# Performance work log

Hardware: AMD Instinct MI355X
Metric: run time of the kernel (lower is better)

Reference implementation:

```python
import jax, jax.numpy as jnp
import numpy as np

B, S, D = 4, 4096, 2048
H, DH = 16, 128
ROPE_BASE = 10000.0


def rotate_half(x):
    x1, x2 = jnp.split(x, 2, axis=-1)
    return jnp.concatenate((-x2, x1), axis=-1)


def rope_cos_sin(seq_len, head_dim, dtype):
    inv_freq = 1.0 / (ROPE_BASE ** (jnp.arange(0, head_dim, 2, dtype=jnp.float32) / head_dim))
    pos = jnp.arange(seq_len, dtype=jnp.float32)
    freqs = pos[:, None] * inv_freq[None, :]          # [S, DH/2]
    emb = jnp.concatenate((freqs, freqs), axis=-1)    # [S, DH]
    return jnp.cos(emb).astype(dtype), jnp.sin(emb).astype(dtype)


def setup_inputs() -> dict:
    key = jax.random.key(0)
    ks = jax.random.split(key, 5)
    scale = 0.02
    return {
        "hidden_states": jax.random.normal(ks[0], (B, S, D), jnp.float32),
        "Wq": jax.random.normal(ks[1], (D, D), jnp.float32) * scale,
        "Wk": jax.random.normal(ks[2], (D, D), jnp.float32) * scale,
        "Wv": jax.random.normal(ks[3], (D, D), jnp.float32) * scale,
        "Wo": jax.random.normal(ks[4], (D, D), jnp.float32) * scale,
    }


def reference(hidden_states, Wq, Wk, Wv, Wo):
    b, s, d = hidden_states.shape
    # QKV projections (nn.Linear stores weight as [out, in] -> x @ W.T)
    def proj(W):
        y = hidden_states @ W.T                       # [B, S, D]
        return y.reshape(b, s, H, DH).transpose(0, 2, 1, 3)  # [B, H, S, DH]
    q, k, v = proj(Wq), proj(Wk), proj(Wv)

    # RoPE (cos/sin broadcast over head dim: unsqueeze_dim=1)
    cos, sin = rope_cos_sin(s, DH, hidden_states.dtype)  # [S, DH]
    cos = cos[None, None]                                # [1, 1, S, DH]
    sin = sin[None, None]
    q = q * cos + rotate_half(q) * sin
    k = k * cos + rotate_half(k) * sin

    # SDPA, non-causal, no mask, eval mode (dropout 0)
    scale = 1.0 / jnp.sqrt(jnp.asarray(DH, hidden_states.dtype))
    scores = jnp.einsum("bhqd,bhkd->bhqk", q, k) * scale
    attn = jax.nn.softmax(scores, axis=-1)
    ctx = jnp.einsum("bhqk,bhkd->bhqd", attn, v)         # [B, H, S, DH]

    ctx = ctx.transpose(0, 2, 1, 3).reshape(b, s, H * DH)
    return ctx @ Wo.T
```

## Files before the change

kernel.cpp:

```cpp
#include <hip/hip_runtime.h>
#include <hip/hip_bf16.h>
#include <math.h>

typedef __attribute__((ext_vector_type(4)))  float f32x4;
typedef __attribute__((ext_vector_type(16))) float f32x16;
typedef __attribute__((ext_vector_type(8)))  short s16x8;
typedef __attribute__((ext_vector_type(4)))  short s16x4;
typedef __attribute__((ext_vector_type(4)))  int   i32x4;

#define DEVI __device__ __forceinline__


DEVI unsigned short f2bf(float x) {
    unsigned int u = __builtin_bit_cast(unsigned int, x);
    u += 0x7fffu + ((u >> 16) & 1u);
    return (unsigned short)(u >> 16);
}

DEVI f32x4 mfma16(s16x8 a, s16x8 b, f32x4 c) {
    return __builtin_amdgcn_mfma_f32_16x16x32_bf16(a, b, c, 0, 0, 0);
}
DEVI f32x16 mfma32(s16x8 a, s16x8 b, f32x16 c) {
    return __builtin_amdgcn_mfma_f32_32x32x16_bf16(a, b, c, 0, 0, 0);
}
DEVI int cvtpk(float lo, float hi) {
    int r; asm("v_cvt_pk_bf16_f32 %0, %1, %2" : "=v"(r) : "v"(lo), "v"(hi)); return r;
}
DEVI void plswap(int& a, int& b) {
    asm volatile("v_permlane32_swap_b32 %0, %1" : "+v"(a), "+v"(b));
}
DEVI void gload16(const void* g, void* l) {
    __builtin_amdgcn_global_load_lds(
        (const __attribute__((address_space(1))) void*)g,
        (__attribute__((address_space(3))) void*)l, 16, 0, 0);
}

__global__ __launch_bounds__(256)
void cvt_kernel(const float* __restrict__ in, unsigned short* __restrict__ out, int n8) {
    int i = blockIdx.x * 256 + threadIdx.x;
    const int stride = gridDim.x * 256;
    for (; i < n8; i += stride) {
        f32x4 a = ((const f32x4*)in)[i * 2];
        f32x4 b = ((const f32x4*)in)[i * 2 + 1];
        s16x8 o;
#pragma unroll
        for (int e = 0; e < 4; ++e) o[e] = (short)f2bf(a[e]);
#pragma unroll
        for (int e = 0; e < 4; ++e) o[4 + e] = (short)f2bf(b[e]);
        *(s16x8*)&out[(size_t)i * 8] = o;
    }
}

__global__ void rope_table_kernel(float* __restrict__ cosb, float* __restrict__ sinb) {
    const int s = blockIdx.x;
    const int i = threadIdx.x;
    const float inv = expf(-(float)i * (9.210340371976184f / 64.0f));
    const float ang = (float)s * inv;
    cosb[s * 64 + i] = cosf(ang);
    sinb[s * 64 + i] = sinf(ang);
}

template <int EPI>
__global__ __launch_bounds__(512, 1)
void gemm8_kernel(const unsigned short* __restrict__ Ah,
                  const unsigned short* __restrict__ Wh,
                  void* __restrict__ Cp, const float* __restrict__ cosb,
                  const float* __restrict__ sinb, float oscale)
{
    constexpr int KD = 2048;
    __shared__ __align__(16) char smem[98304];

    const int tid  = threadIdx.x;
    const int lane = tid & 63;
    const int wid  = tid >> 6;
    const int wm   = wid >> 1;
    const int wn   = wid & 1;
    const int lr   = lane & 15;
    const int lkg  = lane >> 4;
    const int m0   = blockIdx.x * 256;
    const int n0   = blockIdx.y * 128;

    const f32x4 zero4 = {0.f, 0.f, 0.f, 0.f};
    f32x4 acc[4][4];
#pragma unroll
    for (int i = 0; i < 4; ++i)
#pragma unroll
        for (int j = 0; j < 4; ++j) acc[i][j] = zero4;

    const int rsw = (lkg ^ ((lr >> 1) & 3)) << 4;

    auto stageA = [&](int b, int t, int kh) {
        const int k0 = t * 64 + kh * 32;
        char* dst = smem + b * 49152 + kh * 16384;
#pragma unroll
        for (int c = 0; c < 2; ++c) {
            int flat = c * 512 + tid;
            int row  = flat >> 2, slot = flat & 3;
            int sg   = slot ^ ((row >> 1) & 3);
            gload16(&Ah[(size_t)(m0 + row) * KD + k0 + sg * 8], dst + flat * 16);
        }
    };
    auto stageB = [&](int b, int t, int kh) {
        const int k0 = t * 64 + kh * 32;
        char* dst = smem + b * 49152 + 32768 + kh * 8192;
        int row = tid >> 2, slot = tid & 3;
        int sg  = slot ^ ((row >> 1) & 3);
        gload16(&Wh[(size_t)(n0 + row) * KD + k0 + sg * 8], dst + tid * 16);
    };

    auto phase = [&](int b, int ks) {
        const char* Ab = smem + b * 49152 + ks * 16384;
        const char* Bb = smem + b * 49152 + 32768 + ks * 8192;
        s16x8 af[4], bf[4];
#pragma unroll
        for (int mi = 0; mi < 4; ++mi) {
            int row = wm * 64 + mi * 16 + lr;
            af[mi] = *(const s16x8*)(Ab + row * 64 + rsw);
        }
#pragma unroll
        for (int nj = 0; nj < 4; ++nj) {
            int row = wn * 32 + (nj & 1) * 16 + (nj >> 1) * 64 + lr;
            bf[nj] = *(const s16x8*)(Bb + row * 64 + rsw);
        }
        __builtin_amdgcn_s_setprio(1);
#pragma unroll
        for (int mi = 0; mi < 4; ++mi)
#pragma unroll
            for (int nj = 0; nj < 4; ++nj)
                acc[mi][nj] = mfma16(af[mi], bf[nj], acc[mi][nj]);
        __builtin_amdgcn_s_setprio(0);
    };

    stageA(0, 0, 0); stageB(0, 0, 0);
    stageA(0, 0, 1); stageB(0, 0, 1);
    asm volatile("s_waitcnt vmcnt(0)" ::: "memory");
    __builtin_amdgcn_s_barrier();

    for (int t = 0; t < 31; ++t) {
        const int b = t & 1;
        stageA(b ^ 1, t + 1, 0); stageB(b ^ 1, t + 1, 0);
        phase(b, 0);
        asm volatile("s_waitcnt vmcnt(3)" ::: "memory");
        __builtin_amdgcn_s_barrier();
        stageA(b ^ 1, t + 1, 1); stageB(b ^ 1, t + 1, 1);
        phase(b, 1);
        asm volatile("s_waitcnt vmcnt(3)" ::: "memory");
        __builtin_amdgcn_s_barrier();
    }
    phase(1, 0);
    asm volatile("s_waitcnt vmcnt(0)" ::: "memory");
    __builtin_amdgcn_s_barrier();
    phase(1, 1);

    if constexpr (EPI == 0) {
        unsigned short* Qb = (unsigned short*)Cp;
        const int h = blockIdx.y;
#pragma unroll
        for (int mi = 0; mi < 4; ++mi) {
#pragma unroll
            for (int reg = 0; reg < 4; ++reg) {
                int mg = m0 + wm * 64 + mi * 16 + lkg * 4 + reg;
                int bb = mg >> 12, s = mg & 4095;
                size_t base = ((size_t)(bb * 16 + h) * 4096 + s) * 128;
#pragma unroll
                for (int nj = 0; nj < 2; ++nj) {
                    int dlo = wn * 32 + nj * 16 + lr;
                    float cv = cosb[s * 64 + dlo];
                    float sv = sinb[s * 64 + dlo];
                    float a  = acc[mi][nj][reg];
                    float b2 = acc[mi][nj + 2][reg];
                    Qb[base + dlo]      = f2bf((a * cv - b2 * sv) * oscale);
                    Qb[base + dlo + 64] = f2bf((b2 * cv + a * sv) * oscale);
                }
            }
        }
    } else if constexpr (EPI == 1) {
        unsigned short* Vt = (unsigned short*)Cp;
        const int h = blockIdx.y;
        unsigned short* Cs = (unsigned short*)smem;
        __syncthreads();
#pragma unroll
        for (int mi = 0; mi < 4; ++mi)
#pragma unroll
            for (int nj = 0; nj < 4; ++nj) {
                int col = wn * 32 + (nj & 1) * 16 + (nj >> 1) * 64 + lr;
#pragma unroll
                for (int reg = 0; reg < 4; ++reg) {
                    int row = wm * 64 + mi * 16 + lkg * 4 + reg;
                    Cs[row * 136 + col] = f2bf(acc[mi][nj][reg]);
                }
            }
        __syncthreads();
        const int dh = tid >> 2;
        const int sh = (tid & 3) * 64;
        const int bb = m0 >> 12, sbase = m0 & 4095;
        size_t gbase = ((size_t)((bb * 16 + h) * 128 + dh)) * 4096 + sbase + sh;
#pragma unroll
        for (int j0 = 0; j0 < 8; ++j0) {
            s16x8 v;
#pragma unroll
            for (int e = 0; e < 8; ++e)
                v[e] = (short)Cs[(sh + j0 * 8 + e) * 136 + dh];
            *(s16x8*)&Vt[gbase + j0 * 8] = v;
        }
    } else {
        float* Ob = (float*)Cp;
#pragma unroll
        for (int mi = 0; mi < 4; ++mi)
#pragma unroll
            for (int reg = 0; reg < 4; ++reg) {
                int mg = m0 + wm * 64 + mi * 16 + lkg * 4 + reg;
#pragma unroll
                for (int nj = 0; nj < 4; ++nj) {
                    int col = n0 + wn * 32 + (nj & 1) * 16 + (nj >> 1) * 64 + lr;
                    Ob[(size_t)mg * 2048 + col] = acc[mi][nj][reg];
                }
            }
    }
}

template <bool AB16, int EPI>
__global__ __launch_bounds__(256, 2)
void gemm_kernel(const void* __restrict__ Ap, const float* __restrict__ Bw,
                 void* __restrict__ Cp, const float* __restrict__ cosb,
                 const float* __restrict__ sinb, float oscale)
{
    constexpr int KD = 2048;
    __shared__ __align__(16) unsigned short smem[20480];
    unsigned short* const As = smem;
    unsigned short* const Bs = smem + 10240;

    const int tid  = threadIdx.x;
    const int lane = tid & 63;
    const int wid  = tid >> 6;
    const int wr   = wid >> 1, wc = wid & 1;
    const int lr   = lane & 15;
    const int lkg  = lane >> 4;
    const int lk   = lkg * 8;
    const int m0   = blockIdx.x * 128;
    const int n0   = blockIdx.y * 128;

    const f32x4 zero4 = {0.f, 0.f, 0.f, 0.f};
    f32x4 acc[4][4];
#pragma unroll
    for (int i = 0; i < 4; ++i)
#pragma unroll
        for (int j = 0; j < 4; ++j) acc[i][j] = zero4;

    f32x4 aF[4], bF[4];
    s16x8 aH[2];
    const float* Af = (const float*)Ap;
    const unsigned short* AhL = (const unsigned short*)Ap;

    auto stage_load = [&](int kt) {
        const int k0 = kt * 32;
        if constexpr (!AB16) {
#pragma unroll
            for (int i = 0; i < 4; ++i) {
                int flat = i * 256 + tid;
                int r = flat >> 3, c = (flat & 7) * 4;
                aF[i] = *(const f32x4*)&Af[(size_t)(m0 + r) * KD + k0 + c];
            }
        } else {
#pragma unroll
            for (int i = 0; i < 2; ++i) {
                int flat = i * 256 + tid;
                int r = flat >> 2, c = (flat & 3) * 8;
                aH[i] = *(const s16x8*)&AhL[(size_t)(m0 + r) * KD + k0 + c];
            }
        }
#pragma unroll
        for (int i = 0; i < 4; ++i) {
            int flat = i * 256 + tid;
            int r = flat >> 3, c = (flat & 7) * 4;
            bF[i] = *(const f32x4*)&Bw[(size_t)(n0 + r) * KD + k0 + c];
        }
    };
    auto stage_write = [&](int buf) {
        unsigned short* Ab = As + buf * 5120;
        unsigned short* Bb = Bs + buf * 5120;
        if constexpr (!AB16) {
#pragma unroll
            for (int i = 0; i < 4; ++i) {
                int flat = i * 256 + tid;
                int r = flat >> 3, c = (flat & 7) * 4;
                s16x4 v;
#pragma unroll
                for (int e = 0; e < 4; ++e) v[e] = (short)f2bf(aF[i][e]);
                *(s16x4*)&Ab[r * 40 + c] = v;
            }
        } else {
#pragma unroll
            for (int i = 0; i < 2; ++i) {
                int flat = i * 256 + tid;
                int r = flat >> 2, c = (flat & 3) * 8;
                *(s16x8*)&Ab[r * 40 + c] = aH[i];
            }
        }
#pragma unroll
        for (int i = 0; i < 4; ++i) {
            int flat = i * 256 + tid;
            int r = flat >> 3, c = (flat & 7) * 4;
            s16x4 v;
#pragma unroll
            for (int e = 0; e < 4; ++e) v[e] = (short)f2bf(bF[i][e]);
            *(s16x4*)&Bb[r * 40 + c] = v;
        }
    };
    const int ncol0 = wc * 32;
    auto compute = [&](int buf) {
        const unsigned short* Ab = As + buf * 5120;
        const unsigned short* Bb = Bs + buf * 5120;
        s16x8 af[4], bf[4];
#pragma unroll
        for (int mi = 0; mi < 4; ++mi)
            af[mi] = *(const s16x8*)&Ab[(wr * 64 + mi * 16 + lr) * 40 + lk];
#pragma unroll
        for (int nj = 0; nj < 4; ++nj) {
            int nc = ncol0 + (nj & 1) * 16 + (nj >> 1) * 64;
            bf[nj] = *(const s16x8*)&Bb[(nc + lr) * 40 + lk];
        }
#pragma unroll
        for (int mi = 0; mi < 4; ++mi)
#pragma unroll
            for (int nj = 0; nj < 4; ++nj)
                acc[mi][nj] = mfma16(af[mi], bf[nj], acc[mi][nj]);
    };
    stage_load(0);
    stage_write(0);
    __syncthreads();
    for (int kt = 0; kt < 64; ++kt) {
        const int cur = kt & 1;
        if (kt < 63) stage_load(kt + 1);
        compute(cur);
        if (kt < 63) stage_write(cur ^ 1);
        __syncthreads();
    }

    if constexpr (EPI == 0) {
        unsigned short* Qb = (unsigned short*)Cp;
        const int h = blockIdx.y;
#pragma unroll
        for (int mi = 0; mi < 4; ++mi) {
#pragma unroll
            for (int reg = 0; reg < 4; ++reg) {
                int mg = m0 + wr * 64 + mi * 16 + lkg * 4 + reg;
                int bb = mg >> 12, s = mg & 4095;
                size_t base = ((size_t)(bb * 16 + h) * 4096 + s) * 128;
#pragma unroll
                for (int nj = 0; nj < 2; ++nj) {
                    int dlo = wc * 32 + nj * 16 + lr;
                    float cv = cosb[s * 64 + dlo];
                    float sv = sinb[s * 64 + dlo];
                    float a  = acc[mi][nj][reg];
                    float b2 = acc[mi][nj + 2][reg];
                    Qb[base + dlo]      = f2bf((a * cv - b2 * sv) * oscale);
                    Qb[base + dlo + 64] = f2bf((b2 * cv + a * sv) * oscale);
                }
            }
        }
    } else if constexpr (EPI == 1) {
        unsigned short* Vt = (unsigned short*)Cp;
        const int h = blockIdx.y;
        unsigned short* Cs = smem;
        __syncthreads();
#pragma unroll
        for (int mi = 0; mi < 4; ++mi)
#pragma unroll
            for (int nj = 0; nj < 4; ++nj) {
                int col = wc * 32 + (nj & 1) * 16 + (nj >> 1) * 64 + lr;
#pragma unroll
                for (int reg = 0; reg < 4; ++reg) {
                    int row = wr * 64 + mi * 16 + lkg * 4 + reg;
                    Cs[row * 136 + col] = f2bf(acc[mi][nj][reg]);
                }
            }
        __syncthreads();
        const int dh = tid >> 1;
        const int sh = (tid & 1) * 64;
        const int bb = m0 >> 12, sbase = m0 & 4095;
        size_t gbase = ((size_t)((bb * 16 + h) * 128 + dh)) * 4096 + sbase + sh;
#pragma unroll
        for (int j0 = 0; j0 < 8; ++j0) {
            s16x8 v;
#pragma unroll
            for (int e = 0; e < 8; ++e)
                v[e] = (short)Cs[(sh + j0 * 8 + e) * 136 + dh];
            *(s16x8*)&Vt[gbase + j0 * 8] = v;
        }
    } else {
        float* Ob = (float*)Cp;
#pragma unroll
        for (int mi = 0; mi < 4; ++mi)
#pragma unroll
            for (int reg = 0; reg < 4; ++reg) {
                int mg = m0 + wr * 64 + mi * 16 + lkg * 4 + reg;
#pragma unroll
                for (int nj = 0; nj < 4; ++nj) {
                    int col = n0 + wc * 32 + (nj & 1) * 16 + (nj >> 1) * 64 + lr;
                    Ob[(size_t)mg * 2048 + col] = acc[mi][nj][reg];
                }
            }
    }
}

__global__ __launch_bounds__(512, 2)
void attn_kernel(const unsigned short* __restrict__ Q,
                 const unsigned short* __restrict__ Kb,
                 const unsigned short* __restrict__ Vt,
                 unsigned short* __restrict__ ctx)
{
    __shared__ __align__(16) char smem[131072];

    const int tid  = threadIdx.x;
    const int lane = tid & 63;
    const int wid  = tid >> 6;
    const int l31  = lane & 31;
    const int h    = lane >> 5;
    const int qt   = blockIdx.x;
    const int bh   = blockIdx.y;

    const size_t kbase  = (size_t)bh * 4096;
    const size_t vtbase = (size_t)bh * 128 * 4096;

    const size_t qrow = kbase + (size_t)qt * 256 + wid * 32 + l31;
    s16x8 qf[8];
#pragma unroll
    for (int ks = 0; ks < 8; ++ks)
        qf[ks] = *(const s16x8*)&Q[qrow * 128 + ks * 16 + h * 8];

    s16x8 ones;
#pragma unroll
    for (int e = 0; e < 8; ++e) ones[e] = (short)0x3F80;

    const f32x16 Z16 = {0,0,0,0,0,0,0,0,0,0,0,0,0,0,0,0};
    f32x16 accO[4];
    accO[0] = Z16; accO[1] = Z16; accO[2] = Z16; accO[3] = Z16;
    f32x16 accL = Z16;

    auto stage = [&](int buf, int T) {
        const int kv0 = T * 128;
        char* kdst = smem + buf * 65536;
        char* vdst = kdst + 32768;
#pragma unroll
        for (int c = 0; c < 4; ++c) {
            int flat = c * 512 + tid;
            int r    = flat >> 4;
            int col  = (flat & 15) * 16;
            int cs   = col ^ ((r & 15) << 4);
            gload16(&Kb[(kbase + kv0 + r) * 128 + (cs >> 1)], kdst + flat * 16);
            gload16(&Vt[vtbase + (size_t)r * 4096 + kv0 + (cs >> 1)], vdst + flat * 16);
        }
    };

    const int swz   = (l31 & 15) << 4;
    const int hford = wid >> 2;

    stage(0, 0);
    __syncthreads();

    for (int T = 0; T < 32; ++T) {
        const int buf = T & 1;
        if (T < 31) stage(buf ^ 1, T + 1);

        const char* kb = smem + buf * 65536;
        const char* vb = kb + 32768;

#pragma unroll
        for (int hfi = 0; hfi < 2; ++hfi) {
            const int hf = hfi ^ hford;
            const char* kbh = kb + hf * 16384;
            const int   vco = hf * 128;

            f32x16 sc0 = Z16, sc1 = Z16;
            __builtin_amdgcn_s_setprio(1);
#pragma unroll
            for (int ks = 0; ks < 8; ++ks) {
                s16x8 k0 = *(const s16x8*)(kbh + ((l31 * 256 + ks * 32 + h * 16) ^ swz));
                s16x8 k1 = *(const s16x8*)(kbh + (((32 + l31) * 256 + ks * 32 + h * 16) ^ swz));
                sc0 = mfma32(k0, qf[ks], sc0);
                sc1 = mfma32(k1, qf[ks], sc1);
            }
            __builtin_amdgcn_s_setprio(0);

#pragma unroll
            for (int i = 0; i < 16; ++i) sc0[i] = exp2f(sc0[i]);
#pragma unroll
            for (int i = 0; i < 16; ++i) sc1[i] = exp2f(sc1[i]);

            s16x8 pb[4];
#pragma unroll
            for (int g = 0; g < 4; ++g) {
                const f32x16& s = (g < 2) ? sc0 : sc1;
                const int o = (g & 1) * 8;
                int a0 = cvtpk(s[o + 0], s[o + 1]);
                int a1 = cvtpk(s[o + 2], s[o + 3]);
                int b0 = cvtpk(s[o + 4], s[o + 5]);
                int b1 = cvtpk(s[o + 6], s[o + 7]);
                plswap(a0, b0); plswap(a1, b1);
                i32x4 w = {a0, a1, b0, b1};
                pb[g] = __builtin_bit_cast(s16x8, w);
            }

            __builtin_amdgcn_s_setprio(1);
#pragma unroll
            for (int ks = 0; ks < 4; ++ks) {
                accL = mfma32(ones, pb[ks], accL);
#pragma unroll
                for (int mf = 0; mf < 4; ++mf) {
                    s16x8 vf = *(const s16x8*)(vb + ((((mf * 32 + l31) * 256) + (vco + ks * 32 + h * 16)) ^ swz));
                    accO[mf] = mfma32(vf, pb[ks], accO[mf]);
                }
            }
            __builtin_amdgcn_s_setprio(0);
        }

        __syncthreads();
    }

    const float invl = 1.0f / accL[0];
    accO[0] *= invl; accO[1] *= invl; accO[2] *= invl; accO[3] *= invl;

    unsigned short* tw = (unsigned short*)smem + wid * 1088;
    const int bb = bh >> 4, hh = bh & 15;
    const size_t cbase = ((size_t)(bb * 4096 + qt * 256 + wid * 32 + l31)) * 2048 + hh * 128;
#pragma unroll
    for (int mf = 0; mf < 4; ++mf) {
#pragma unroll
        for (int reg = 0; reg < 16; ++reg) {
            int d = (reg & 3) + 8 * (reg >> 2) + 4 * h;
            tw[d * 34 + l31] = f2bf(accO[mf][reg]);
        }
        s16x8 o0, o1;
#pragma unroll
        for (int dd = 0; dd < 8; ++dd) {
            o0[dd] = (short)tw[(h * 16 + dd) * 34 + l31];
            o1[dd] = (short)tw[(h * 16 + 8 + dd) * 34 + l31];
        }
        *(s16x8*)&ctx[cbase + mf * 32 + h * 16]     = o0;
        *(s16x8*)&ctx[cbase + mf * 32 + h * 16 + 8] = o1;
    }
}

extern "C" void kernel_launch(void* const* d_in, const int* in_sizes, int n_in,
                              void* d_out, int out_size, void* d_ws, size_t ws_size,
                              hipStream_t stream)
{
    (void)in_sizes; (void)n_in; (void)out_size;
    const float* X  = (const float*)d_in[0];
    const float* Wq = (const float*)d_in[1];
    const float* Wk = (const float*)d_in[2];
    const float* Wv = (const float*)d_in[3];
    const float* Wo = (const float*)d_in[4];

    char* ws = (char*)d_ws;
    const size_t TBL  = 2097152;
    const size_t HBUF = 67108864;
    const size_t WBUF = 8388608;
    const size_t SX   = 33554432;
    const size_t SW   = 4194304;

    float* cosb = (float*)ws;
    float* sinb = (float*)(ws + 1048576);

    const float QSCALE = 0.12751763f;
    dim3 g8(64, 16), blk8(512), blk(256);

    rope_table_kernel<<<dim3(4096), dim3(64), 0, stream>>>(cosb, sinb);

    if (ws_size >= TBL + HBUF + 4 * WBUF + 4 * HBUF) {
        unsigned short* Xb  = (unsigned short*)(ws + TBL);
        unsigned short* Wb0 = (unsigned short*)(ws + TBL + HBUF);
        unsigned short* Qb  = (unsigned short*)(ws + TBL + HBUF + 4 * WBUF);
        unsigned short* Kb  = Qb + SX;
        unsigned short* Vtb = Kb + SX;
        unsigned short* Cb  = Vtb + SX;
        const float* Wsrc[4] = {Wq, Wk, Wv, Wo};
        cvt_kernel<<<dim3(2048), blk, 0, stream>>>(X, Xb, (int)(SX / 8));
        for (int w = 0; w < 4; ++w)
            cvt_kernel<<<dim3(1024), blk, 0, stream>>>(Wsrc[w], Wb0 + w * SW, (int)(SW / 8));
        gemm8_kernel<0><<<g8, blk8, 0, stream>>>(Xb, Wb0,          Qb, cosb, sinb, QSCALE);
        gemm8_kernel<0><<<g8, blk8, 0, stream>>>(Xb, Wb0 + SW,     Kb, cosb, sinb, 1.0f);
        gemm8_kernel<1><<<g8, blk8, 0, stream>>>(Xb, Wb0 + 2 * SW, Vtb, cosb, sinb, 1.0f);
        attn_kernel<<<dim3(16, 64), dim3(512), 0, stream>>>(Qb, Kb, Vtb, Cb);
        gemm8_kernel<2><<<g8, blk8, 0, stream>>>(Cb, Wb0 + 3 * SW, d_out, cosb, sinb, 1.0f);
    } else if (ws_size >= TBL + HBUF + 4 * WBUF + HBUF) {
        unsigned short* Xb  = (unsigned short*)(ws + TBL);
        unsigned short* Wb0 = (unsigned short*)(ws + TBL + HBUF);
        unsigned short* Vtb = (unsigned short*)(ws + TBL + HBUF + 4 * WBUF);
        unsigned short* Qb  = (unsigned short*)d_out;
        unsigned short* Kb  = Qb + SX;
        unsigned short* Cb  = Xb;
        const float* Wsrc[4] = {Wq, Wk, Wv, Wo};
        cvt_kernel<<<dim3(2048), blk, 0, stream>>>(X, Xb, (int)(SX / 8));
        for (int w = 0; w < 4; ++w)
            cvt_kernel<<<dim3(1024), blk, 0, stream>>>(Wsrc[w], Wb0 + w * SW, (int)(SW / 8));
        gemm8_kernel<0><<<g8, blk8, 0, stream>>>(Xb, Wb0,          Qb, cosb, sinb, QSCALE);
        gemm8_kernel<0><<<g8, blk8, 0, stream>>>(Xb, Wb0 + SW,     Kb, cosb, sinb, 1.0f);
        gemm8_kernel<1><<<g8, blk8, 0, stream>>>(Xb, Wb0 + 2 * SW, Vtb, cosb, sinb, 1.0f);
        attn_kernel<<<dim3(16, 64), dim3(512), 0, stream>>>(Qb, Kb, Vtb, Cb);
        gemm8_kernel<2><<<g8, blk8, 0, stream>>>(Cb, Wb0 + 3 * SW, d_out, cosb, sinb, 1.0f);
    } else {
        unsigned short* Vtb = (unsigned short*)(ws + TBL);
        unsigned short* Cb  = (unsigned short*)(ws + TBL + HBUF);
        unsigned short* Qb  = (unsigned short*)d_out;
        unsigned short* Kb  = Qb + SX;
        dim3 gg(128, 16);
        gemm_kernel<false, 0><<<gg, blk, 0, stream>>>(X, Wq, Qb, cosb, sinb, QSCALE);
        gemm_kernel<false, 0><<<gg, blk, 0, stream>>>(X, Wk, Kb, cosb, sinb, 1.0f);
        gemm_kernel<false, 1><<<gg, blk, 0, stream>>>(X, Wv, Vtb, cosb, sinb, 1.0f);
        attn_kernel<<<dim3(16, 64), dim3(512), 0, stream>>>(Qb, Kb, Vtb, Cb);
        gemm_kernel<true, 2><<<gg, blk, 0, stream>>>(Cb, Wo, d_out, cosb, sinb, 1.0f);
    }
}
```

Measured before the change: 1.326 ms.

## Widen projection GEMM tiles to 256x256 and interleave B loads with MFMA phases

The bf16 projection GEMM goes from 256x128 to 256x256 output tiles per 512-thread block. Each wave now holds 4x8 accumulators and covers a full head pair, and the grid shrinks to 64x8. The goal is more arithmetic per byte loaded from global memory and LDS, fewer blocks, and each block's B-load staging split between two MFMA half-phases to overlap loads with compute. The cost is 128 KB of shared memory, more accumulator registers, and a V-transpose epilogue that now runs in two serialized passes.

Measured after the change: 1.178 ms. 11.1% less time.

```diff
diff --git a/kernel.cpp b/kernel.cpp
--- a/kernel.cpp
+++ b/kernel.cpp
@@ -62,13 +62,13 @@
 
 template <int EPI>
 __global__ __launch_bounds__(512, 1)
-void gemm8_kernel(const unsigned short* __restrict__ Ah,
-                  const unsigned short* __restrict__ Wh,
-                  void* __restrict__ Cp, const float* __restrict__ cosb,
-                  const float* __restrict__ sinb, float oscale)
+void gemm256_kernel(const unsigned short* __restrict__ Ah,
+                    const unsigned short* __restrict__ Wh,
+                    void* __restrict__ Cp, const float* __restrict__ cosb,
+                    const float* __restrict__ sinb, float oscale)
 {
     constexpr int KD = 2048;
-    __shared__ __align__(16) char smem[98304];
+    __shared__ __align__(16) char smem[131072];
 
     const int tid  = threadIdx.x;
     const int lane = tid & 63;
@@ -78,20 +78,20 @@
     const int lr   = lane & 15;
     const int lkg  = lane >> 4;
     const int m0   = blockIdx.x * 256;
-    const int n0   = blockIdx.y * 128;
+    const int n0   = blockIdx.y * 256;
 
     const f32x4 zero4 = {0.f, 0.f, 0.f, 0.f};
-    f32x4 acc[4][4];
+    f32x4 acc[4][8];
 #pragma unroll
     for (int i = 0; i < 4; ++i)
 #pragma unroll
-        for (int j = 0; j < 4; ++j) acc[i][j] = zero4;
+        for (int j = 0; j < 8; ++j) acc[i][j] = zero4;
 
     const int rsw = (lkg ^ ((lr >> 1) & 3)) << 4;
 
     auto stageA = [&](int b, int t, int kh) {
         const int k0 = t * 64 + kh * 32;
-        char* dst = smem + b * 49152 + kh * 16384;
+        char* dst = smem + b * 65536 + kh * 16384;
 #pragma unroll
         for (int c = 0; c < 2; ++c) {
             int flat = c * 512 + tid;
@@ -102,15 +102,19 @@
     };
     auto stageB = [&](int b, int t, int kh) {
         const int k0 = t * 64 + kh * 32;
-        char* dst = smem + b * 49152 + 32768 + kh * 8192;
-        int row = tid >> 2, slot = tid & 3;
-        int sg  = slot ^ ((row >> 1) & 3);
-        gload16(&Wh[(size_t)(n0 + row) * KD + k0 + sg * 8], dst + tid * 16);
+        char* dst = smem + b * 65536 + 32768 + kh * 16384;
+#pragma unroll
+        for (int c = 0; c < 2; ++c) {
+            int flat = c * 512 + tid;
+            int row  = flat >> 2, slot = flat & 3;
+            int sg   = slot ^ ((row >> 1) & 3);
+            gload16(&Wh[(size_t)(n0 + row) * KD + k0 + sg * 8], dst + flat * 16);
+        }
     };
 
-    auto phase = [&](int b, int ks) {
-        const char* Ab = smem + b * 49152 + ks * 16384;
-        const char* Bb = smem + b * 49152 + 32768 + ks * 8192;
+    auto phase = [&](int b, int ks, int ng) {
+        const char* Ab = smem + b * 65536 + ks * 16384;
+        const char* Bb = smem + b * 65536 + 32768 + ks * 16384;
         s16x8 af[4], bf[4];
 #pragma unroll
         for (int mi = 0; mi < 4; ++mi) {
@@ -118,16 +122,16 @@
             af[mi] = *(const s16x8*)(Ab + row * 64 + rsw);
         }
 #pragma unroll
-        for (int nj = 0; nj < 4; ++nj) {
-            int row = wn * 32 + (nj & 1) * 16 + (nj >> 1) * 64 + lr;
-            bf[nj] = *(const s16x8*)(Bb + row * 64 + rsw);
+        for (int j = 0; j < 4; ++j) {
+            int row = wn * 128 + ng * 64 + j * 16 + lr;
+            bf[j] = *(const s16x8*)(Bb + row * 64 + rsw);
         }
         __builtin_amdgcn_s_setprio(1);
 #pragma unroll
         for (int mi = 0; mi < 4; ++mi)
 #pragma unroll
-            for (int nj = 0; nj < 4; ++nj)
-                acc[mi][nj] = mfma16(af[mi], bf[nj], acc[mi][nj]);
+            for (int j = 0; j < 4; ++j)
+                acc[mi][ng * 4 + j] = mfma16(af[mi], bf[j], acc[mi][ng * 4 + j]);
         __builtin_amdgcn_s_setprio(0);
     };
 
@@ -138,23 +142,27 @@
 
     for (int t = 0; t < 31; ++t) {
         const int b = t & 1;
-        stageA(b ^ 1, t + 1, 0); stageB(b ^ 1, t + 1, 0);
-        phase(b, 0);
-        asm volatile("s_waitcnt vmcnt(3)" ::: "memory");
+        stageA(b ^ 1, t + 1, 0);
+        phase(b, 0, 0);
+        stageB(b ^ 1, t + 1, 0);
+        phase(b, 0, 1);
+        asm volatile("s_waitcnt vmcnt(4)" ::: "memory");
         __builtin_amdgcn_s_barrier();
-        stageA(b ^ 1, t + 1, 1); stageB(b ^ 1, t + 1, 1);
-        phase(b, 1);
-        asm volatile("s_waitcnt vmcnt(3)" ::: "memory");
+        stageA(b ^ 1, t + 1, 1);
+        phase(b, 1, 0);
+        stageB(b ^ 1, t + 1, 1);
+        phase(b, 1, 1);
+        asm volatile("s_waitcnt vmcnt(4)" ::: "memory");
         __builtin_amdgcn_s_barrier();
     }
-    phase(1, 0);
+    phase(1, 0, 0); phase(1, 0, 1);
     asm volatile("s_waitcnt vmcnt(0)" ::: "memory");
     __builtin_amdgcn_s_barrier();
-    phase(1, 1);
+    phase(1, 1, 0); phase(1, 1, 1);
 
     if constexpr (EPI == 0) {
         unsigned short* Qb = (unsigned short*)Cp;
-        const int h = blockIdx.y;
+        const int h = blockIdx.y * 2 + wn;
 #pragma unroll
         for (int mi = 0; mi < 4; ++mi) {
 #pragma unroll
@@ -163,12 +171,12 @@
                 int bb = mg >> 12, s = mg & 4095;
                 size_t base = ((size_t)(bb * 16 + h) * 4096 + s) * 128;
 #pragma unroll
-                for (int nj = 0; nj < 2; ++nj) {
-                    int dlo = wn * 32 + nj * 16 + lr;
+                for (int nj = 0; nj < 4; ++nj) {
+                    int dlo = nj * 16 + lr;
                     float cv = cosb[s * 64 + dlo];
                     float sv = sinb[s * 64 + dlo];
                     float a  = acc[mi][nj][reg];
-                    float b2 = acc[mi][nj + 2][reg];
+                    float b2 = acc[mi][nj + 4][reg];
                     Qb[base + dlo]      = f2bf((a * cv - b2 * sv) * oscale);
                     Qb[base + dlo + 64] = f2bf((b2 * cv + a * sv) * oscale);
                 }
@@ -176,32 +184,37 @@
         }
     } else if constexpr (EPI == 1) {
         unsigned short* Vt = (unsigned short*)Cp;
-        const int h = blockIdx.y;
         unsigned short* Cs = (unsigned short*)smem;
-        __syncthreads();
-#pragma unroll
-        for (int mi = 0; mi < 4; ++mi)
-#pragma unroll
-            for (int nj = 0; nj < 4; ++nj) {
-                int col = wn * 32 + (nj & 1) * 16 + (nj >> 1) * 64 + lr;
-#pragma unroll
-                for (int reg = 0; reg < 4; ++reg) {
-                    int row = wm * 64 + mi * 16 + lkg * 4 + reg;
-                    Cs[row * 136 + col] = f2bf(acc[mi][nj][reg]);
-                }
-            }
-        __syncthreads();
-        const int dh = tid >> 2;
-        const int sh = (tid & 3) * 64;
         const int bb = m0 >> 12, sbase = m0 & 4095;
-        size_t gbase = ((size_t)((bb * 16 + h) * 128 + dh)) * 4096 + sbase + sh;
-#pragma unroll
-        for (int j0 = 0; j0 < 8; ++j0) {
-            s16x8 v;
-#pragma unroll
-            for (int e = 0; e < 8; ++e)
-                v[e] = (short)Cs[(sh + j0 * 8 + e) * 136 + dh];
-            *(s16x8*)&Vt[gbase + j0 * 8] = v;
+#pragma unroll
+        for (int p = 0; p < 2; ++p) {
+            __syncthreads();
+            if (wn == p) {
+#pragma unroll
+                for (int mi = 0; mi < 4; ++mi)
+#pragma unroll
+                    for (int nj = 0; nj < 8; ++nj) {
+                        int col = (nj & 3) * 16 + (nj >> 2) * 64 + lr;
+#pragma unroll
+                        for (int reg = 0; reg < 4; ++reg) {
+                            int row = wm * 64 + mi * 16 + lkg * 4 + reg;
+                            Cs[row * 136 + col] = f2bf(acc[mi][nj][reg]);
+                        }
+                    }
+            }
+            __syncthreads();
+            const int h  = blockIdx.y * 2 + p;
+            const int dh = tid >> 2;
+            const int sh = (tid & 3) * 64;
+            size_t gbase = ((size_t)((bb * 16 + h) * 128 + dh)) * 4096 + sbase + sh;
+#pragma unroll
+            for (int j0 = 0; j0 < 8; ++j0) {
+                s16x8 v;
+#pragma unroll
+                for (int e = 0; e < 8; ++e)
+                    v[e] = (short)Cs[(sh + j0 * 8 + e) * 136 + dh];
+                *(s16x8*)&Vt[gbase + j0 * 8] = v;
+            }
         }
     } else {
         float* Ob = (float*)Cp;
@@ -211,8 +224,8 @@
             for (int reg = 0; reg < 4; ++reg) {
                 int mg = m0 + wm * 64 + mi * 16 + lkg * 4 + reg;
 #pragma unroll
-                for (int nj = 0; nj < 4; ++nj) {
-                    int col = n0 + wn * 32 + (nj & 1) * 16 + (nj >> 1) * 64 + lr;
+                for (int nj = 0; nj < 8; ++nj) {
+                    int col = n0 + wn * 128 + (nj & 3) * 16 + (nj >> 2) * 64 + lr;
                     Ob[(size_t)mg * 2048 + col] = acc[mi][nj][reg];
                 }
             }
@@ -564,7 +577,7 @@
     float* sinb = (float*)(ws + 1048576);
 
     const float QSCALE = 0.12751763f;
-    dim3 g8(64, 16), blk8(512), blk(256);
+    dim3 g8(64, 8), blk8(512), blk(256);
 
     rope_table_kernel<<<dim3(4096), dim3(64), 0, stream>>>(cosb, sinb);
 
@@ -579,11 +592,11 @@
         cvt_kernel<<<dim3(2048), blk, 0, stream>>>(X, Xb, (int)(SX / 8));
         for (int w = 0; w < 4; ++w)
             cvt_kernel<<<dim3(1024), blk, 0, stream>>>(Wsrc[w], Wb0 + w * SW, (int)(SW / 8));
-        gemm8_kernel<0><<<g8, blk8, 0, stream>>>(Xb, Wb0,          Qb, cosb, sinb, QSCALE);
-        gemm8_kernel<0><<<g8, blk8, 0, stream>>>(Xb, Wb0 + SW,     Kb, cosb, sinb, 1.0f);
-        gemm8_kernel<1><<<g8, blk8, 0, stream>>>(Xb, Wb0 + 2 * SW, Vtb, cosb, sinb, 1.0f);
+        gemm256_kernel<0><<<g8, blk8, 0, stream>>>(Xb, Wb0,          Qb, cosb, sinb, QSCALE);
+        gemm256_kernel<0><<<g8, blk8, 0, stream>>>(Xb, Wb0 + SW,     Kb, cosb, sinb, 1.0f);
+        gemm256_kernel<1><<<g8, blk8, 0, stream>>>(Xb, Wb0 + 2 * SW, Vtb, cosb, sinb, 1.0f);
         attn_kernel<<<dim3(16, 64), dim3(512), 0, stream>>>(Qb, Kb, Vtb, Cb);
-        gemm8_kernel<2><<<g8, blk8, 0, stream>>>(Cb, Wb0 + 3 * SW, d_out, cosb, sinb, 1.0f);
+        gemm256_kernel<2><<<g8, blk8, 0, stream>>>(Cb, Wb0 + 3 * SW, d_out, cosb, sinb, 1.0f);
     } else if (ws_size >= TBL + HBUF + 4 * WBUF + HBUF) {
         unsigned short* Xb  = (unsigned short*)(ws + TBL);
         unsigned short* Wb0 = (unsigned short*)(ws + TBL + HBUF);
@@ -595,11 +608,11 @@
         cvt_kernel<<<dim3(2048), blk, 0, stream>>>(X, Xb, (int)(SX / 8));
         for (int w = 0; w < 4; ++w)
             cvt_kernel<<<dim3(1024), blk, 0, stream>>>(Wsrc[w], Wb0 + w * SW, (int)(SW / 8));
-        gemm8_kernel<0><<<g8, blk8, 0, stream>>>(Xb, Wb0,          Qb, cosb, sinb, QSCALE);
-        gemm8_kernel<0><<<g8, blk8, 0, stream>>>(Xb, Wb0 + SW,     Kb, cosb, sinb, 1.0f);
-        gemm8_kernel<1><<<g8, blk8, 0, stream>>>(Xb, Wb0 + 2 * SW, Vtb, cosb, sinb, 1.0f);
+        gemm256_kernel<0><<<g8, blk8, 0, stream>>>(Xb, Wb0,          Qb, cosb, sinb, QSCALE);
+        gemm256_kernel<0><<<g8, blk8, 0, stream>>>(Xb, Wb0 + SW,     Kb, cosb, sinb, 1.0f);
+        gemm256_kernel<1><<<g8, blk8, 0, stream>>>(Xb, Wb0 + 2 * SW, Vtb, cosb, sinb, 1.0f);
         attn_kernel<<<dim3(16, 64), dim3(512), 0, stream>>>(Qb, Kb, Vtb, Cb);
-        gemm8_kernel<2><<<g8, blk8, 0, stream>>>(Cb, Wb0 + 3 * SW, d_out, cosb, sinb, 1.0f);
+        gemm256_kernel<2><<<g8, blk8, 0, stream>>>(Cb, Wb0 + 3 * SW, d_out, cosb, sinb, 1.0f);
     } else {
         unsigned short* Vtb = (unsigned short*)(ws + TBL);
         unsigned short* Cb  = (unsigned short*)(ws + TBL + HBUF);
```
